# Optimization experiments

Measured on AMD Instinct MI355X. Metric: run time of the kernel, lower is better.

Reference implementation:

```python
import jax, jax.numpy as jnp
import numpy as np

TEMP = 0.2
EPS = 1e-12


def _l2norm(v, axis=1):
    n = jnp.linalg.norm(v, axis=axis, keepdims=True)
    return v / jnp.maximum(n, EPS)


def setup_inputs() -> dict:
    key = jax.random.key(0)
    ks = jax.random.split(key, 7)
    B, D, P, K = 2048, 256, 100, 30
    return {
        "x": jax.random.normal(ks[0], (B, D), jnp.float32),
        "x_aug": jax.random.normal(ks[1], (B, D), jnp.float32),
        "proto_w": jax.random.normal(ks[2], (P, D), jnp.float32),
        "hard_q1": jax.random.randint(ks[3], (B,), 0, P, jnp.int32),
        "hard_q2": jax.random.randint(ks[4], (B,), 0, P, jnp.int32),
        "neg_q1": jax.random.randint(ks[5], (B, K), 0, P, jnp.int32),
        "neg_q2": jax.random.randint(ks[6], (B, K), 0, P, jnp.int32),
    }


def reference(x, x_aug, proto_w, hard_q1, hard_q2, neg_q1, neg_q2):
    B = x.shape[0]
    N = 2 * B
    P = proto_w.shape[0]

    out1 = _l2norm(x)                          # [B, D]
    out2 = _l2norm(x_aug)                      # [B, D]
    out = jnp.concatenate([out1, out2], axis=0)  # [N, D]
    hard_q = jnp.concatenate([hard_q1, hard_q2], axis=0)  # [N]
    neg_q = jnp.concatenate([neg_q1, neg_q2], axis=0)     # [N, K]

    sim = jnp.exp(jnp.matmul(out, out.T) / TEMP)  # [N, N]
    eye = jnp.eye(N, dtype=bool)

    # hard_selection: mask[i,j] = (i != j) and (hard_q[j] in neg_q[i])
    # build per-row prototype membership table [N, P] to avoid a [N, K, N] blowup
    member = jnp.zeros((N, P), dtype=bool).at[jnp.arange(N)[:, None], neg_q].set(True)
    mask = (~eye) & member[:, hard_q]  # member[i, hard_q[j]] -> [N, N]

    # sample_reweighting
    w = _l2norm(proto_w)                # normalized prototypes [P, D]
    proto_dist = jnp.matmul(w, w.T)     # cosine similarity [P, P]
    R = proto_dist[hard_q[:, None], hard_q[None, :]]  # [N, N]
    R = jnp.where(eye, 0.0, R)          # diag is 0 when the row min is taken
    rmin = jnp.min(R, axis=1, keepdims=True)
    R = jnp.where(eye, rmin, R)         # reweight[i][i] = min(reweight[i])
    rmax = jnp.max(R, axis=1, keepdims=True)
    R = (R - rmin) / (rmax - rmin)      # per-row min-max normalize
    mu = jnp.mean(R, axis=1, keepdims=True)
    std = jnp.std(R, axis=1, ddof=1, keepdims=True)  # torch.std is unbiased
    reweight = jnp.exp((R - mu) ** 2 / (2.0 * std ** 2))
    sim = sim * reweight

    # masked_select(...).sum() == global sum over masked entries (scalar)
    total = jnp.sum(jnp.where(mask, sim, 0.0))

    pos = jnp.exp(jnp.sum(out1 * out2, axis=-1) / TEMP)  # [B]
    pos = jnp.concatenate([pos, pos], axis=0)            # [N]
    loss = jnp.mean(-jnp.log(pos / total))
    return loss
```

## Files before the change

kernel.cpp:

```cpp
#include <hip/hip_runtime.h>
#include <hip/hip_bf16.h>
#include <cstdint>

#define B_ 2048
#define N_ 4096
#define D_ 256
#define P_ 100
#define K_ 30
#define INVT 5.0f

typedef __attribute__((ext_vector_type(8))) short bf16x8;
typedef __attribute__((ext_vector_type(4))) float f32x4;
typedef __attribute__((ext_vector_type(4))) unsigned short us4;

__device__ __forceinline__ float waveReduceSum(float v) {
#pragma unroll
  for (int off = 32; off > 0; off >>= 1) v += __shfl_xor(v, off, 64);
  return v;
}

__device__ __forceinline__ unsigned short f2bf(float f) {
  __hip_bfloat16 h = __float2bfloat16(f);
  return *reinterpret_cast<unsigned short*>(&h);
}
__device__ __forceinline__ float bf2f(unsigned short u) {
  return __uint_as_float(((unsigned int)u) << 16);
}

__global__ __launch_bounds__(256) void prep_kernel(
    const float* __restrict__ x, const float* __restrict__ xa, const float* __restrict__ pw,
    const int* __restrict__ hq1, const int* __restrict__ hq2, int* __restrict__ hq,
    int* __restrict__ cnt, float* __restrict__ pd, __hip_bfloat16* __restrict__ outb,
    float* __restrict__ sums) {
  __shared__ int c[P_];
  __shared__ float s4[4];
  int t = threadIdx.x, lane = t & 63, wv = t >> 6;
  int bx = blockIdx.x;
  if (bx == 0) {
    if (t < 2) sums[t] = 0.f;
    if (t == 2) ((int*)sums)[2] = 0;
    if (t < P_) c[t] = 0;
    __syncthreads();
    for (int i = t; i < N_; i += 256) {
      int q = (i < B_) ? hq1[i] : hq2[i - B_];
      hq[i] = q;
      atomicAdd(&c[q], 1);
    }
    __syncthreads();
    if (t < P_) cnt[t] = c[t];
  } else if (bx <= P_) {
    int q = bx - 1;
    float4 aq = ((const float4*)(pw + q * D_))[lane];
    float ssq = waveReduceSum(aq.x * aq.x + aq.y * aq.y + aq.z * aq.z + aq.w * aq.w);
    float qinv = 1.f / fmaxf(sqrtf(ssq), 1e-12f);
    for (int r = wv; r < P_; r += 4) {
      float4 b = ((const float4*)(pw + r * D_))[lane];
      float s = aq.x * b.x + aq.y * b.y + aq.z * b.z + aq.w * b.w;
      float n = b.x * b.x + b.y * b.y + b.z * b.z + b.w * b.w;
      s = waveReduceSum(s);
      n = waveReduceSum(n);
      if (lane == 0) pd[q * P_ + r] = s * qinv / fmaxf(sqrtf(n), 1e-12f);
    }
  } else {
    int i = (bx - 101) * 4 + wv;
    float4 a = ((const float4*)(x + i * D_))[lane];
    float ss = waveReduceSum(a.x * a.x + a.y * a.y + a.z * a.z + a.w * a.w);
    float inv1 = 1.f / fmaxf(sqrtf(ss), 1e-12f);
    float o1x = a.x * inv1, o1y = a.y * inv1, o1z = a.z * inv1, o1w = a.w * inv1;
    us4 p1; p1[0] = f2bf(o1x); p1[1] = f2bf(o1y); p1[2] = f2bf(o1z); p1[3] = f2bf(o1w);
    ((us4*)(outb + i * D_))[lane] = p1;
    float4 b = ((const float4*)(xa + i * D_))[lane];
    float ss2 = waveReduceSum(b.x * b.x + b.y * b.y + b.z * b.z + b.w * b.w);
    float inv2 = 1.f / fmaxf(sqrtf(ss2), 1e-12f);
    float o2x = b.x * inv2, o2y = b.y * inv2, o2z = b.z * inv2, o2w = b.w * inv2;
    us4 p2; p2[0] = f2bf(o2x); p2[1] = f2bf(o2y); p2[2] = f2bf(o2z); p2[3] = f2bf(o2w);
    ((us4*)(outb + (B_ + i) * D_))[lane] = p2;
    float d = waveReduceSum(o1x * o2x + o1y * o2y + o1z * o2z + o1w * o2w);
    if (lane == 0) s4[wv] = d;
    __syncthreads();
    if (t == 0) atomicAdd(&sums[1], s4[0] + s4[1] + s4[2] + s4[3]);
  }
}

__global__ void gtab_kernel(const int* __restrict__ hq, const int* __restrict__ cnt,
                            const float* __restrict__ pd, const int* __restrict__ nq1,
                            const int* __restrict__ nq2, unsigned short* __restrict__ gtabh) {
  __shared__ unsigned char memb[4][104];
  int wv = threadIdx.x >> 6, lane = threadIdx.x & 63;
  int i = blockIdx.x * 4 + wv;
  int q = hq[i];
  if (lane < 52) { memb[wv][lane * 2] = 0; memb[wv][lane * 2 + 1] = 0; }
  __syncthreads();
  const int* nrow = (i < B_) ? (nq1 + i * K_) : (nq2 + (i - B_) * K_);
  if (lane < K_) memb[wv][nrow[lane]] = 1;
  __syncthreads();

  int p0 = lane, p1 = lane + 64;
  bool has1 = (p1 < P_);
  float v0 = pd[q * P_ + p0];
  int m0 = cnt[p0] - (p0 == q ? 1 : 0);
  float v1 = 0.f; int m1 = 0;
  if (has1) { v1 = pd[q * P_ + p1]; m1 = cnt[p1] - (p1 == q ? 1 : 0); }

  float mn = 1e30f, mx = -1e30f;
  if (m0 > 0) { mn = fminf(mn, v0); mx = fmaxf(mx, v0); }
  if (has1 && m1 > 0) { mn = fminf(mn, v1); mx = fmaxf(mx, v1); }
#pragma unroll
  for (int off = 32; off > 0; off >>= 1) {
    mn = fminf(mn, __shfl_xor(mn, off, 64));
    mx = fmaxf(mx, __shfl_xor(mx, off, 64));
  }
  float rmin = fminf(0.f, mn);
  float rmax = fmaxf(rmin, mx);
  float inv = 1.f / (rmax - rmin);
  float r0 = (v0 - rmin) * inv, r1 = (v1 - rmin) * inv;
  float s1 = (m0 > 0 ? (float)m0 * r0 : 0.f) + ((has1 && m1 > 0) ? (float)m1 * r1 : 0.f);
  s1 = waveReduceSum(s1);
  float mu = s1 / (float)N_;
  float ss = (m0 > 0 ? (float)m0 * (r0 - mu) * (r0 - mu) : 0.f) +
             ((has1 && m1 > 0) ? (float)m1 * (r1 - mu) * (r1 - mu) : 0.f);
  ss = waveReduceSum(ss);
  ss += mu * mu;
  float var = ss / (float)(N_ - 1);
  float i2v = 1.f / (2.f * var);
  float g0 = memb[wv][p0] ? __expf((r0 - mu) * (r0 - mu) * i2v) : 0.f;
  gtabh[i * P_ + p0] = f2bf(g0);
  if (has1) {
    float g1 = memb[wv][p1] ? __expf((r1 - mu) * (r1 - mu) * i2v) : 0.f;
    gtabh[i * P_ + p1] = f2bf(g1);
  }
}

__device__ __forceinline__ void gload16(void* ldsdst, const void* gsrc) {
  __builtin_amdgcn_global_load_lds(
      (const __attribute__((address_space(1))) unsigned int*)gsrc,
      (__attribute__((address_space(3))) unsigned int*)ldsdst, 16, 0, 0);
}

__global__ __launch_bounds__(512, 4) void tot_kernel(
    const __hip_bfloat16* __restrict__ outb, const unsigned short* __restrict__ gtabh,
    const int* __restrict__ hq, float* __restrict__ sums, float* __restrict__ out) {
  __shared__ __align__(16) char lds[65536];
  __shared__ float s8[8];
  const int tid = threadIdx.x, lane = tid & 63, wid = tid >> 6;
  const int i0 = blockIdx.y * 128, j0 = blockIdx.x * 128;
  const int wr = wid >> 2, wc = wid & 3;

  f32x4 acc[4][2] = {};

  const int wseg = wid & 3;
  const bool isB = (wid >= 4);
  const int growbase = isB ? j0 : i0;
  char* panel = lds + (isB ? 32768 : 0);

  for (int kk = 0; kk < 2; ++kk) {
#pragma unroll
    for (int it = 0; it < 8; ++it) {
      int rbase = wseg * 32 + it * 4;
      int row = rbase + (lane >> 4);
      int c = lane & 15;
      int src = (growbase + row) * D_ + kk * 128 + ((c ^ (row & 7)) * 8);
      gload16(panel + rbase * 256, outb + src);
    }
    __syncthreads();
#pragma unroll
    for (int ks = 0; ks < 4; ++ks) {
      bf16x8 af[4], bfr[2];
#pragma unroll
      for (int m = 0; m < 4; ++m) {
        int row = wr * 64 + m * 16 + (lane & 15);
        int off = row * 256 + ((((ks << 2) + (lane >> 4)) ^ (row & 7)) << 4);
        af[m] = *(const bf16x8*)(lds + off);
      }
#pragma unroll
      for (int n = 0; n < 2; ++n) {
        int row = wc * 32 + n * 16 + (lane & 15);
        int off = 32768 + row * 256 + ((((ks << 2) + (lane >> 4)) ^ (row & 7)) << 4);
        bfr[n] = *(const bf16x8*)(lds + off);
      }
#pragma unroll
      for (int m = 0; m < 4; ++m)
#pragma unroll
        for (int n = 0; n < 2; ++n)
          acc[m][n] = __builtin_amdgcn_mfma_f32_16x16x32_bf16(af[m], bfr[n], acc[m][n], 0, 0, 0);
    }
    __syncthreads();
  }

  unsigned short* gaT = (unsigned short*)lds;
  int* hqj = (int*)(lds + 26624);
  for (int idx = tid; idx < 128 * P_; idx += 512) {
    int r = idx / P_, c = idx - r * P_;
    gaT[c * 132 + r] = gtabh[(i0 + r) * P_ + c];
  }
  if (tid < 128) hqj[tid] = hq[j0 + tid];
  __syncthreads();

  const int jl0 = wc * 32 + (lane & 15);
  const int jl1 = jl0 + 16;
  const int hj0 = hqj[jl0], hj1 = hqj[jl1];
  const int jg0 = j0 + jl0, jg1 = j0 + jl1;
  float local = 0.f;
#pragma unroll
  for (int m = 0; m < 4; ++m) {
    int ilb = wr * 64 + m * 16 + ((lane >> 4) << 2);
    us4 w0 = *(const us4*)(gaT + hj0 * 132 + ilb);
    us4 w1 = *(const us4*)(gaT + hj1 * 132 + ilb);
#pragma unroll
    for (int r = 0; r < 4; ++r) {
      int ig = i0 + ilb + r;
      float e0 = __expf(acc[m][0][r] * INVT);
      float e1 = __expf(acc[m][1][r] * INVT);
      local += (ig != jg0) ? bf2f(w0[r]) * e0 : 0.f;
      local += (ig != jg1) ? bf2f(w1[r]) * e1 : 0.f;
    }
  }
  local = waveReduceSum(local);
  if (lane == 0) s8[wid] = local;
  __syncthreads();
  if (tid == 0) {
    float t = 0.f;
#pragma unroll
    for (int w = 0; w < 8; ++w) t += s8[w];
    atomicAdd(&sums[0], t);
    __threadfence();
    int* ticket = (int*)sums + 2;
    int done = atomicAdd(ticket, 1);
    if (done == 1023) {
      float tot = atomicAdd(&sums[0], 0.f);
      float pos = atomicAdd(&sums[1], 0.f);
      out[0] = logf(tot) - pos * (INVT / (float)B_);
    }
  }
}

extern "C" void kernel_launch(void* const* d_in, const int* in_sizes, int n_in,
                              void* d_out, int out_size, void* d_ws, size_t ws_size,
                              hipStream_t stream) {
  const float* x   = (const float*)d_in[0];
  const float* xa  = (const float*)d_in[1];
  const float* pw  = (const float*)d_in[2];
  const int* hq1   = (const int*)d_in[3];
  const int* hq2   = (const int*)d_in[4];
  const int* nq1   = (const int*)d_in[5];
  const int* nq2   = (const int*)d_in[6];
  float* out = (float*)d_out;

  char* ws = (char*)d_ws;
  __hip_bfloat16* outb  = (__hip_bfloat16*)(ws);
  unsigned short* gtabh = (unsigned short*)(ws + 2097152);
  float* pd    = (float*)(ws + 2916352);
  int*   hq    = (int*)  (ws + 2956800);
  int*   cnt   = (int*)  (ws + 2973184);
  float* sums  = (float*)(ws + 2973696);

  prep_kernel<<<613, 256, 0, stream>>>(x, xa, pw, hq1, hq2, hq, cnt, pd, outb, sums);
  gtab_kernel<<<N_ / 4, 256, 0, stream>>>(hq, cnt, pd, nq1, nq2, gtabh);
  tot_kernel<<<dim3(32, 32), 512, 0, stream>>>(outb, gtabh, hq, sums, out);
}
```

Baseline: 132.7 us.

## Exploit Gram-matrix symmetry with upper-triangular 64x64 single-wave tiles

Replaces the 128x128, 8-wave LDS-staged GEMM tiles with 64x64 tiles handled by a single wave. Only the upper-triangular tile pairs are launched, and for each off-diagonal tile the weights from both the (i,j) and (j,i) entries are summed, since exp(sim) is symmetric. Operands now load straight from global memory into registers with double buffering, so no LDS is used, and the reweight table is read directly from global. This roughly halves the MFMA and exp work. In exchange it adds scattered global gathers from gtabh, issues more atomics and skips the LDS reuse.

```diff
diff --git a/kernel.cpp b/kernel.cpp
--- a/kernel.cpp
+++ b/kernel.cpp
@@ -8,6 +8,8 @@
 #define P_ 100
 #define K_ 30
 #define INVT 5.0f
+#define NTILE 64
+#define NJOBS (NTILE * (NTILE + 1) / 2)
 
 typedef __attribute__((ext_vector_type(8))) short bf16x8;
 typedef __attribute__((ext_vector_type(4))) float f32x4;
@@ -131,102 +133,92 @@
   }
 }
 
-__device__ __forceinline__ void gload16(void* ldsdst, const void* gsrc) {
-  __builtin_amdgcn_global_load_lds(
-      (const __attribute__((address_space(1))) unsigned int*)gsrc,
-      (__attribute__((address_space(3))) unsigned int*)ldsdst, 16, 0, 0);
-}
-
-__global__ __launch_bounds__(512, 4) void tot_kernel(
+__global__ __launch_bounds__(64) void tot_kernel(
     const __hip_bfloat16* __restrict__ outb, const unsigned short* __restrict__ gtabh,
     const int* __restrict__ hq, float* __restrict__ sums, float* __restrict__ out) {
-  __shared__ __align__(16) char lds[65536];
-  __shared__ float s8[8];
-  const int tid = threadIdx.x, lane = tid & 63, wid = tid >> 6;
-  const int i0 = blockIdx.y * 128, j0 = blockIdx.x * 128;
-  const int wr = wid >> 2, wc = wid & 3;
-
-  f32x4 acc[4][2] = {};
-
-  const int wseg = wid & 3;
-  const bool isB = (wid >= 4);
-  const int growbase = isB ? j0 : i0;
-  char* panel = lds + (isB ? 32768 : 0);
-
-  for (int kk = 0; kk < 2; ++kk) {
-#pragma unroll
-    for (int it = 0; it < 8; ++it) {
-      int rbase = wseg * 32 + it * 4;
-      int row = rbase + (lane >> 4);
-      int c = lane & 15;
-      int src = (growbase + row) * D_ + kk * 128 + ((c ^ (row & 7)) * 8);
-      gload16(panel + rbase * 256, outb + src);
-    }
-    __syncthreads();
-#pragma unroll
-    for (int ks = 0; ks < 4; ++ks) {
-      bf16x8 af[4], bfr[2];
+  const int lane = threadIdx.x;
+  const int r16 = lane & 15, k8 = lane >> 4;
+
+  int rem = blockIdx.x, ti = 0;
+  while (rem >= NTILE - ti) { rem -= NTILE - ti; ++ti; }
+  const int tj = ti + rem;
+  const bool diag = (ti == tj);
+  const int i0 = ti * 64, j0 = tj * 64;
+
+  const __hip_bfloat16* Ab = outb + (i0 + r16) * D_ + k8 * 8;
+  const __hip_bfloat16* Bb = outb + (j0 + r16) * D_ + k8 * 8;
+
+  f32x4 acc[4][4] = {};
+  bf16x8 a[2][4], b[2][4];
+#pragma unroll
+  for (int m = 0; m < 4; ++m) {
+    a[0][m] = *(const bf16x8*)(Ab + m * 16 * D_);
+    b[0][m] = *(const bf16x8*)(Bb + m * 16 * D_);
+  }
+#pragma unroll
+  for (int kk = 0; kk < 8; ++kk) {
+    const int cur = kk & 1, nxt = cur ^ 1;
+    if (kk < 7) {
 #pragma unroll
       for (int m = 0; m < 4; ++m) {
-        int row = wr * 64 + m * 16 + (lane & 15);
-        int off = row * 256 + ((((ks << 2) + (lane >> 4)) ^ (row & 7)) << 4);
-        af[m] = *(const bf16x8*)(lds + off);
+        a[nxt][m] = *(const bf16x8*)(Ab + m * 16 * D_ + (kk + 1) * 32);
+        b[nxt][m] = *(const bf16x8*)(Bb + m * 16 * D_ + (kk + 1) * 32);
       }
-#pragma unroll
-      for (int n = 0; n < 2; ++n) {
-        int row = wc * 32 + n * 16 + (lane & 15);
-        int off = 32768 + row * 256 + ((((ks << 2) + (lane >> 4)) ^ (row & 7)) << 4);
-        bfr[n] = *(const bf16x8*)(lds + off);
+    }
+#pragma unroll
+    for (int m = 0; m < 4; ++m)
+#pragma unroll
+      for (int n = 0; n < 4; ++n)
+        acc[m][n] = __builtin_amdgcn_mfma_f32_16x16x32_bf16(a[cur][m], b[cur][n], acc[m][n], 0, 0, 0);
+  }
+
+  int4 hi4[4];
+#pragma unroll
+  for (int m = 0; m < 4; ++m) hi4[m] = *(const int4*)(hq + i0 + m * 16 + k8 * 4);
+  int hj[4];
+#pragma unroll
+  for (int n = 0; n < 4; ++n) hj[n] = hq[j0 + n * 16 + r16];
+
+  float local = 0.f;
+  if (diag) {
+#pragma unroll
+    for (int m = 0; m < 4; ++m) {
+#pragma unroll
+      for (int n = 0; n < 4; ++n) {
+#pragma unroll
+        for (int r = 0; r < 4; ++r) {
+          int il = m * 16 + k8 * 4 + r;
+          int jl = n * 16 + r16;
+          float e = __expf(acc[m][n][r] * INVT);
+          float wv = bf2f(gtabh[(i0 + il) * P_ + hj[n]]);
+          if (il != jl) local += wv * e;
+        }
       }
-#pragma unroll
-      for (int m = 0; m < 4; ++m)
-#pragma unroll
-        for (int n = 0; n < 2; ++n)
-          acc[m][n] = __builtin_amdgcn_mfma_f32_16x16x32_bf16(af[m], bfr[n], acc[m][n], 0, 0, 0);
-    }
-    __syncthreads();
-  }
-
-  unsigned short* gaT = (unsigned short*)lds;
-  int* hqj = (int*)(lds + 26624);
-  for (int idx = tid; idx < 128 * P_; idx += 512) {
-    int r = idx / P_, c = idx - r * P_;
-    gaT[c * 132 + r] = gtabh[(i0 + r) * P_ + c];
-  }
-  if (tid < 128) hqj[tid] = hq[j0 + tid];
-  __syncthreads();
-
-  const int jl0 = wc * 32 + (lane & 15);
-  const int jl1 = jl0 + 16;
-  const int hj0 = hqj[jl0], hj1 = hqj[jl1];
-  const int jg0 = j0 + jl0, jg1 = j0 + jl1;
-  float local = 0.f;
-#pragma unroll
-  for (int m = 0; m < 4; ++m) {
-    int ilb = wr * 64 + m * 16 + ((lane >> 4) << 2);
-    us4 w0 = *(const us4*)(gaT + hj0 * 132 + ilb);
-    us4 w1 = *(const us4*)(gaT + hj1 * 132 + ilb);
-#pragma unroll
-    for (int r = 0; r < 4; ++r) {
-      int ig = i0 + ilb + r;
-      float e0 = __expf(acc[m][0][r] * INVT);
-      float e1 = __expf(acc[m][1][r] * INVT);
-      local += (ig != jg0) ? bf2f(w0[r]) * e0 : 0.f;
-      local += (ig != jg1) ? bf2f(w1[r]) * e1 : 0.f;
+    }
+  } else {
+#pragma unroll
+    for (int m = 0; m < 4; ++m) {
+#pragma unroll
+      for (int n = 0; n < 4; ++n) {
+#pragma unroll
+        for (int r = 0; r < 4; ++r) {
+          int i = i0 + m * 16 + k8 * 4 + r;
+          int j = j0 + n * 16 + r16;
+          float e = __expf(acc[m][n][r] * INVT);
+          float wv = bf2f(gtabh[i * P_ + hj[n]]);
+          int hi = ((const int*)&hi4[m])[r];
+          wv += bf2f(gtabh[j * P_ + hi]);
+          local += wv * e;
+        }
+      }
     }
   }
   local = waveReduceSum(local);
-  if (lane == 0) s8[wid] = local;
-  __syncthreads();
-  if (tid == 0) {
-    float t = 0.f;
-#pragma unroll
-    for (int w = 0; w < 8; ++w) t += s8[w];
-    atomicAdd(&sums[0], t);
+  if (lane == 0) {
+    atomicAdd(&sums[0], local);
     __threadfence();
-    int* ticket = (int*)sums + 2;
-    int done = atomicAdd(ticket, 1);
-    if (done == 1023) {
+    int done = atomicAdd((int*)sums + 2, 1);
+    if (done == NJOBS - 1) {
       float tot = atomicAdd(&sums[0], 0.f);
       float pos = atomicAdd(&sums[1], 0.f);
       out[0] = logf(tot) - pos * (INVT / (float)B_);
@@ -256,5 +248,5 @@
 
   prep_kernel<<<613, 256, 0, stream>>>(x, xa, pw, hq1, hq2, hq, cnt, pd, outb, sums);
   gtab_kernel<<<N_ / 4, 256, 0, stream>>>(hq, cnt, pd, nq1, nq2, gtabh);
-  tot_kernel<<<dim3(32, 32), 512, 0, stream>>>(outb, gtabh, hq, sums, out);
-}
+  tot_kernel<<<NJOBS, 64, 0, stream>>>(outb, gtabh, hq, sums, out);
+}
```

New measurement: 170.3 us. 1.28x slower.
